# Kernel tuning notes

Measured on AMD Instinct MI355X. Metric: run time of the kernel, lower is better.

The kernel has to match this reference:

```python
import jax, jax.numpy as jnp
import numpy as np

DIM = 64  # QK head dim, matches init kwarg 'dim'

def setup_inputs() -> dict:
    key = jax.random.key(0)
    kq, kk, kv = jax.random.split(key, 3)
    B, L, C, D, H = 2, 2048, 16, DIM, 64
    query = jax.random.normal(kq, (B, L, C, D), dtype=jnp.float32)
    k_ = jax.random.normal(kk, (B, L, C, D), dtype=jnp.float32)
    value = jax.random.normal(kv, (B, L, C, H), dtype=jnp.float32)
    return {"query": query, "key": k_, "value": value}

def reference(query, key, value):
    scaler = 1.0 / jnp.sqrt(jnp.float32(DIM))
    # score: [b, c, l, m]
    score = jnp.einsum('blcd,bmcd->bclm', query, key) * scaler
    # mask=False, dropout=0 -> identity
    attn = jax.nn.softmax(score, axis=3)
    # out: [b, l, c, h]
    out = jnp.einsum('bmch,bclm->blch', value, attn)
    return out
```

## Files before the change

kernel.cpp:

```cpp
#include <hip/hip_runtime.h>
#include <hip/hip_bf16.h>
#include <stdint.h>

#define B_ 2
#define L_ 2048
#define C_ 16
#define D_ 64
#define H_ 64
#define QBLK 128
#define KVBLK 64
#define NTILES 32
#define NTHREADS 256
#define NHEADS 32
#define TILE_ELEMS 4096
#define TENSOR_ELEMS (NHEADS * NTILES * TILE_ELEMS)

typedef __attribute__((ext_vector_type(8))) short bf16x8;
typedef __attribute__((ext_vector_type(16))) float f32x16;
typedef __attribute__((ext_vector_type(8))) unsigned short u16x8;

__device__ inline unsigned short f2bf(float f) {
  union { float f; unsigned int u; } v; v.f = f;
  unsigned int u = v.u;
  unsigned int r = (u + 0x7FFFu + ((u >> 16) & 1u)) >> 16;
  return (unsigned short)r;
}

__device__ inline float fast_exp2(float x) {
#if __has_builtin(__builtin_amdgcn_exp2f)
  return __builtin_amdgcn_exp2f(x);
#else
  return exp2f(x);
#endif
}

__device__ inline unsigned cvt_pk_bf16(float lo, float hi) {
  unsigned r;
  asm("v_cvt_pk_bf16_f32 %0, %1, %2" : "=v"(r) : "v"(lo), "v"(hi));
  return r;
}

__device__ inline void pl32swap(unsigned &x, unsigned &y) {
#if __has_builtin(__builtin_amdgcn_permlane32_swap)
  auto r = __builtin_amdgcn_permlane32_swap(x, y, false, false);
  x = r[0]; y = r[1];
#else
  asm("v_permlane32_swap_b32 %0, %1" : "+v"(x), "+&v"(y));
#endif
}

__device__ inline float xsum32(float v) {
  unsigned x = __float_as_uint(v), y = x;
  pl32swap(x, y);
  return __uint_as_float(x) + __uint_as_float(y);
}

__global__ __launch_bounds__(256) void prepack_kernel(
    const float* __restrict__ Kg, const float* __restrict__ Vg,
    unsigned short* __restrict__ Kb, unsigned short* __restrict__ Vb) {
  int idx = blockIdx.x * 256 + threadIdx.x;
  if (idx < 524288) {
    int i = idx;
    int lane = i & 63, frag = (i >> 6) & 7, t = (i >> 9) & 31, head = i >> 14;
    int b = head >> 4, c = head & 15;
    int ks = frag >> 1, half = frag & 1;
    int row = half * 32 + (lane & 31);
    int kb = ks * 16 + (lane >> 5) * 8;
    const float* src = Kg + ((size_t)(b * L_ + t * 64 + row) * C_ + c) * D_ + kb;
    float4 a0 = ((const float4*)src)[0];
    float4 a1 = ((const float4*)src)[1];
    u16x8 pk;
    pk[0] = f2bf(a0.x); pk[1] = f2bf(a0.y); pk[2] = f2bf(a0.z); pk[3] = f2bf(a0.w);
    pk[4] = f2bf(a1.x); pk[5] = f2bf(a1.y); pk[6] = f2bf(a1.z); pk[7] = f2bf(a1.w);
    size_t dst = ((((size_t)(head * 32 + t)) * 8 + frag) * 64 + lane) * 8;
    *(u16x8*)&Kb[dst] = pk;
  } else {
    int i = idx - 524288;
    int lane = i & 63, frag = (i >> 6) & 7, t = (i >> 9) & 31, head = i >> 14;
    int b = head >> 4, c = head & 15;
    int m = frag >> 1, half = frag & 1;
    int h = half * 32 + (lane & 31);
    int kv0 = m * 16 + (lane >> 5) * 8;
    const float* src = Vg + ((size_t)(b * L_ + t * 64 + kv0) * C_ + c) * H_ + h;
    u16x8 pv;
#pragma unroll
    for (int j = 0; j < 8; ++j) pv[j] = f2bf(src[(size_t)j * C_ * H_]);
    size_t dst = ((((size_t)(head * 32 + t)) * 8 + frag) * 64 + lane) * 8;
    *(u16x8*)&Vb[dst] = pv;
  }
}

#define SM(S0, S1, PF, L)                                                         \
  {                                                                               \
    float rst[4];                                                                 \
    _Pragma("unroll")                                                             \
    for (int tq = 0; tq < 4; ++tq) {                                              \
      const int be = ((2 * tq) & 3) * 4;                                          \
      const int bo = ((2 * tq + 1) & 3) * 4;                                      \
      float p0[4], p1[4];                                                         \
      _Pragma("unroll")                                                           \
      for (int r = 0; r < 4; ++r) {                                               \
        float se = (tq < 2) ? S0[be + r] : S1[be + r];                            \
        float so_ = (tq < 2) ? S0[bo + r] : S1[bo + r];                           \
        p0[r] = fast_exp2(se);                                                    \
        p1[r] = fast_exp2(so_);                                                   \
      }                                                                           \
      rst[tq] = ((p0[0] + p0[1]) + (p0[2] + p0[3])) +                             \
                ((p1[0] + p1[1]) + (p1[2] + p1[3]));                              \
      unsigned x0 = cvt_pk_bf16(p0[0], p0[1]);                                    \
      unsigned x1 = cvt_pk_bf16(p0[2], p0[3]);                                    \
      unsigned y0 = cvt_pk_bf16(p1[0], p1[1]);                                    \
      unsigned y1 = cvt_pk_bf16(p1[2], p1[3]);                                    \
      pl32swap(x0, y0);                                                           \
      pl32swap(x1, y1);                                                           \
      union { unsigned wd[4]; bf16x8 v; } pk_;                                    \
      pk_.wd[0] = x0; pk_.wd[1] = x1; pk_.wd[2] = y0; pk_.wd[3] = y1;             \
      PF[tq] = pk_.v;                                                             \
    }                                                                             \
    L += (rst[0] + rst[1]) + (rst[2] + rst[3]);                                   \
  }

__global__ __launch_bounds__(NTHREADS, 2) void attn_fwd_kernel(
    const float* __restrict__ Qg,
    const unsigned short* __restrict__ Kb,
    const unsigned short* __restrict__ Vb,
    float* __restrict__ Og) {
  __shared__ float Osh[2 * 64 * 68];
  __shared__ float lsh[2 * 2 * 64];

  const int tid  = threadIdx.x;
  const int lane = tid & 63;
  const int w    = tid >> 6;
  const int qw   = w >> 1;
  const int g    = w & 1;
  const int ql   = lane & 31;
  const int u    = lane >> 5;

  const int bid   = blockIdx.x;
  const int swz   = (bid & 7) * 64 + (bid >> 3);
  const int head  = swz >> 4;
  const int qtile = swz & 15;
  const int b     = head >> 4;
  const int c     = head & 15;
  const int q0    = qtile * QBLK + qw * 64;

  const unsigned short* KbL = Kb + (size_t)head * NTILES * TILE_ELEMS + lane * 8;
  const unsigned short* VbL = Vb + (size_t)head * NTILES * TILE_ELEMS + lane * 8;

  const float sc2 = 0.125f * 1.44269504088896340736f;
  bf16x8 qf0[4], qf1[4];
#pragma unroll
  for (int h = 0; h < 2; ++h) {
    const int qr = q0 + h * 32 + ql;
    const float* qrow = Qg + ((size_t)(b * L_ + qr) * C_ + c) * D_;
#pragma unroll
    for (int ks = 0; ks < 4; ++ks) {
      float4 a0 = *(const float4*)(qrow + ks * 16 + u * 8);
      float4 a1 = *(const float4*)(qrow + ks * 16 + u * 8 + 4);
      bf16x8 q8;
      q8[0] = (short)f2bf(a0.x * sc2); q8[1] = (short)f2bf(a0.y * sc2);
      q8[2] = (short)f2bf(a0.z * sc2); q8[3] = (short)f2bf(a0.w * sc2);
      q8[4] = (short)f2bf(a1.x * sc2); q8[5] = (short)f2bf(a1.y * sc2);
      q8[6] = (short)f2bf(a1.z * sc2); q8[7] = (short)f2bf(a1.w * sc2);
      if (h == 0) qf0[ks] = q8; else qf1[ks] = q8;
    }
  }

  f32x16 o00, o01, o10, o11;
#pragma unroll
  for (int i = 0; i < 16; ++i) { o00[i] = 0.f; o01[i] = 0.f; o10[i] = 0.f; o11[i] = 0.f; }
  float l0 = 0.f, l1 = 0.f;

  bf16x8 ka0, ka1, ka2, ka3;
  {
    const unsigned short* K0 = KbL + (size_t)g * TILE_ELEMS;
    ka0 = *(const bf16x8*)(K0);
    ka1 = *(const bf16x8*)(K0 + 512);
    ka2 = *(const bf16x8*)(K0 + 1024);
    ka3 = *(const bf16x8*)(K0 + 1536);
  }

  for (int tt = 0; tt < NTILES / 2; ++tt) {
    const int t = g + 2 * tt;
    const int tn = (tt + 1 < NTILES / 2) ? t + 2 : t;
    const unsigned short* Kt = KbL + (size_t)t * TILE_ELEMS;
    const unsigned short* Vt = VbL + (size_t)t * TILE_ELEMS;
    const unsigned short* Kn = KbL + (size_t)tn * TILE_ELEMS;

    f32x16 s00, s01, s10, s11;
#pragma unroll
    for (int i = 0; i < 16; ++i) { s00[i] = 0.f; s01[i] = 0.f; s10[i] = 0.f; s11[i] = 0.f; }

    bf16x8 kb0 = *(const bf16x8*)(Kt + 2048);
    bf16x8 kb1 = *(const bf16x8*)(Kt + 2560);
    bf16x8 kb2 = *(const bf16x8*)(Kt + 3072);
    bf16x8 kb3 = *(const bf16x8*)(Kt + 3584);
    __builtin_amdgcn_s_setprio(1);
    s00 = __builtin_amdgcn_mfma_f32_32x32x16_bf16(ka0, qf0[0], s00, 0, 0, 0);
    s01 = __builtin_amdgcn_mfma_f32_32x32x16_bf16(ka1, qf0[0], s01, 0, 0, 0);
    s10 = __builtin_amdgcn_mfma_f32_32x32x16_bf16(ka0, qf1[0], s10, 0, 0, 0);
    s11 = __builtin_amdgcn_mfma_f32_32x32x16_bf16(ka1, qf1[0], s11, 0, 0, 0);
    s00 = __builtin_amdgcn_mfma_f32_32x32x16_bf16(ka2, qf0[1], s00, 0, 0, 0);
    s01 = __builtin_amdgcn_mfma_f32_32x32x16_bf16(ka3, qf0[1], s01, 0, 0, 0);
    s10 = __builtin_amdgcn_mfma_f32_32x32x16_bf16(ka2, qf1[1], s10, 0, 0, 0);
    s11 = __builtin_amdgcn_mfma_f32_32x32x16_bf16(ka3, qf1[1], s11, 0, 0, 0);
    __builtin_amdgcn_s_setprio(0);

    ka0 = *(const bf16x8*)(Vt);
    ka1 = *(const bf16x8*)(Vt + 512);
    ka2 = *(const bf16x8*)(Vt + 1024);
    ka3 = *(const bf16x8*)(Vt + 1536);
    __builtin_amdgcn_s_setprio(1);
    s00 = __builtin_amdgcn_mfma_f32_32x32x16_bf16(kb0, qf0[2], s00, 0, 0, 0);
    s01 = __builtin_amdgcn_mfma_f32_32x32x16_bf16(kb1, qf0[2], s01, 0, 0, 0);
    s10 = __builtin_amdgcn_mfma_f32_32x32x16_bf16(kb0, qf1[2], s10, 0, 0, 0);
    s11 = __builtin_amdgcn_mfma_f32_32x32x16_bf16(kb1, qf1[2], s11, 0, 0, 0);
    s00 = __builtin_amdgcn_mfma_f32_32x32x16_bf16(kb2, qf0[3], s00, 0, 0, 0);
    s01 = __builtin_amdgcn_mfma_f32_32x32x16_bf16(kb3, qf0[3], s01, 0, 0, 0);
    s10 = __builtin_amdgcn_mfma_f32_32x32x16_bf16(kb2, qf1[3], s10, 0, 0, 0);
    s11 = __builtin_amdgcn_mfma_f32_32x32x16_bf16(kb3, qf1[3], s11, 0, 0, 0);
    __builtin_amdgcn_s_setprio(0);

    kb0 = *(const bf16x8*)(Vt + 2048);
    kb1 = *(const bf16x8*)(Vt + 2560);
    kb2 = *(const bf16x8*)(Vt + 3072);
    kb3 = *(const bf16x8*)(Vt + 3584);
    bf16x8 pf0[4], pf1[4];
    SM(s00, s01, pf0, l0);
    SM(s10, s11, pf1, l1);

    __builtin_amdgcn_s_setprio(1);
    o00 = __builtin_amdgcn_mfma_f32_32x32x16_bf16(ka0, pf0[0], o00, 0, 0, 0);
    o01 = __builtin_amdgcn_mfma_f32_32x32x16_bf16(ka1, pf0[0], o01, 0, 0, 0);
    o10 = __builtin_amdgcn_mfma_f32_32x32x16_bf16(ka0, pf1[0], o10, 0, 0, 0);
    o11 = __builtin_amdgcn_mfma_f32_32x32x16_bf16(ka1, pf1[0], o11, 0, 0, 0);
    o00 = __builtin_amdgcn_mfma_f32_32x32x16_bf16(ka2, pf0[1], o00, 0, 0, 0);
    o01 = __builtin_amdgcn_mfma_f32_32x32x16_bf16(ka3, pf0[1], o01, 0, 0, 0);
    o10 = __builtin_amdgcn_mfma_f32_32x32x16_bf16(ka2, pf1[1], o10, 0, 0, 0);
    o11 = __builtin_amdgcn_mfma_f32_32x32x16_bf16(ka3, pf1[1], o11, 0, 0, 0);
    __builtin_amdgcn_s_setprio(0);

    ka0 = *(const bf16x8*)(Kn);
    ka1 = *(const bf16x8*)(Kn + 512);
    ka2 = *(const bf16x8*)(Kn + 1024);
    ka3 = *(const bf16x8*)(Kn + 1536);
    __builtin_amdgcn_s_setprio(1);
    o00 = __builtin_amdgcn_mfma_f32_32x32x16_bf16(kb0, pf0[2], o00, 0, 0, 0);
    o01 = __builtin_amdgcn_mfma_f32_32x32x16_bf16(kb1, pf0[2], o01, 0, 0, 0);
    o10 = __builtin_amdgcn_mfma_f32_32x32x16_bf16(kb0, pf1[2], o10, 0, 0, 0);
    o11 = __builtin_amdgcn_mfma_f32_32x32x16_bf16(kb1, pf1[2], o11, 0, 0, 0);
    o00 = __builtin_amdgcn_mfma_f32_32x32x16_bf16(kb2, pf0[3], o00, 0, 0, 0);
    o01 = __builtin_amdgcn_mfma_f32_32x32x16_bf16(kb3, pf0[3], o01, 0, 0, 0);
    o10 = __builtin_amdgcn_mfma_f32_32x32x16_bf16(kb2, pf1[3], o10, 0, 0, 0);
    o11 = __builtin_amdgcn_mfma_f32_32x32x16_bf16(kb3, pf1[3], o11, 0, 0, 0);
    __builtin_amdgcn_s_setprio(0);
  }

  float la0 = xsum32(l0), la1 = xsum32(l1);
  float* Ow = &Osh[(qw * 64 + lane) * 68];
  if (g == 1) {
#pragma unroll
    for (int rg = 0; rg < 4; ++rg) {
      *(float4*)(Ow + rg * 4)      = (float4){o00[rg*4+0], o00[rg*4+1], o00[rg*4+2], o00[rg*4+3]};
      *(float4*)(Ow + 16 + rg * 4) = (float4){o01[rg*4+0], o01[rg*4+1], o01[rg*4+2], o01[rg*4+3]};
      *(float4*)(Ow + 32 + rg * 4) = (float4){o10[rg*4+0], o10[rg*4+1], o10[rg*4+2], o10[rg*4+3]};
      *(float4*)(Ow + 48 + rg * 4) = (float4){o11[rg*4+0], o11[rg*4+1], o11[rg*4+2], o11[rg*4+3]};
    }
    lsh[(qw * 2 + 0) * 64 + lane] = la0;
    lsh[(qw * 2 + 1) * 64 + lane] = la1;
  }
  __syncthreads();
  if (g == 0) {
    const float inv0 = 1.0f / (la0 + lsh[(qw * 2 + 0) * 64 + lane]);
    const float inv1 = 1.0f / (la1 + lsh[(qw * 2 + 1) * 64 + lane]);
    const int qr0 = q0 + ql;
    const int qr1 = q0 + 32 + ql;
    float* orow0 = Og + ((size_t)(b * L_ + qr0) * C_ + c) * H_;
    float* orow1 = Og + ((size_t)(b * L_ + qr1) * C_ + c) * H_;
#pragma unroll
    for (int rg = 0; rg < 4; ++rg) {
      float4 a0 = *(const float4*)(Ow + rg * 4);
      float4 a1 = *(const float4*)(Ow + 16 + rg * 4);
      float4 a2 = *(const float4*)(Ow + 32 + rg * 4);
      float4 a3 = *(const float4*)(Ow + 48 + rg * 4);
      float4 v0, v1, v2, v3;
      v0.x = (o00[rg*4+0] + a0.x) * inv0; v0.y = (o00[rg*4+1] + a0.y) * inv0;
      v0.z = (o00[rg*4+2] + a0.z) * inv0; v0.w = (o00[rg*4+3] + a0.w) * inv0;
      v1.x = (o01[rg*4+0] + a1.x) * inv0; v1.y = (o01[rg*4+1] + a1.y) * inv0;
      v1.z = (o01[rg*4+2] + a1.z) * inv0; v1.w = (o01[rg*4+3] + a1.w) * inv0;
      v2.x = (o10[rg*4+0] + a2.x) * inv1; v2.y = (o10[rg*4+1] + a2.y) * inv1;
      v2.z = (o10[rg*4+2] + a2.z) * inv1; v2.w = (o10[rg*4+3] + a2.w) * inv1;
      v3.x = (o11[rg*4+0] + a3.x) * inv1; v3.y = (o11[rg*4+1] + a3.y) * inv1;
      v3.z = (o11[rg*4+2] + a3.z) * inv1; v3.w = (o11[rg*4+3] + a3.w) * inv1;
      *(float4*)(orow0 + 8 * rg + 4 * u) = v0;
      *(float4*)(orow0 + 32 + 8 * rg + 4 * u) = v1;
      *(float4*)(orow1 + 8 * rg + 4 * u) = v2;
      *(float4*)(orow1 + 32 + 8 * rg + 4 * u) = v3;
    }
  }
}

extern "C" void kernel_launch(void* const* d_in, const int* in_sizes, int n_in,
                              void* d_out, int out_size, void* d_ws, size_t ws_size,
                              hipStream_t stream) {
  const float* Qg = (const float*)d_in[0];
  const float* Kg = (const float*)d_in[1];
  const float* Vg = (const float*)d_in[2];
  float* Og = (float*)d_out;

  unsigned short* Kb = (unsigned short*)d_ws;
  unsigned short* Vb = Kb + (size_t)TENSOR_ELEMS;

  prepack_kernel<<<4096, 256, 0, stream>>>(Kg, Vg, Kb, Vb);

  dim3 grid(NHEADS * (L_ / QBLK));
  dim3 block(NTHREADS);
  attn_fwd_kernel<<<grid, block, 0, stream>>>(Qg, Kb, Vb, Og);
}
```

Baseline: 57.87 us.

## Halve query block to 64 rows per block for more blocks and occupancy

Each wave now handles 32 query rows instead of 64, so the block covers 64 queries and the grid doubles to 1024 blocks. Accumulator and score registers are halved, launch bounds are raised to 3 blocks per SIMD, and the grid swizzle and shared-memory reduction buffers are resized. The aim is more parallelism and latency hiding, at the cost of each K/V tile being reloaded from L2 by twice as many blocks and less MFMA work per load.

```diff
diff --git a/kernel.cpp b/kernel.cpp
--- a/kernel.cpp
+++ b/kernel.cpp
@@ -7,7 +7,7 @@
 #define C_ 16
 #define D_ 64
 #define H_ 64
-#define QBLK 128
+#define QBLK 64
 #define KVBLK 64
 #define NTILES 32
 #define NTHREADS 256
@@ -120,13 +120,13 @@
     L += (rst[0] + rst[1]) + (rst[2] + rst[3]);                                   \
   }
 
-__global__ __launch_bounds__(NTHREADS, 2) void attn_fwd_kernel(
+__global__ __launch_bounds__(NTHREADS, 3) void attn_fwd_kernel(
     const float* __restrict__ Qg,
     const unsigned short* __restrict__ Kb,
     const unsigned short* __restrict__ Vb,
     float* __restrict__ Og) {
-  __shared__ float Osh[2 * 64 * 68];
-  __shared__ float lsh[2 * 2 * 64];
+  __shared__ float Osh[2 * 64 * 36];
+  __shared__ float lsh[2 * 64];
 
   const int tid  = threadIdx.x;
   const int lane = tid & 63;
@@ -137,39 +137,36 @@
   const int u    = lane >> 5;
 
   const int bid   = blockIdx.x;
-  const int swz   = (bid & 7) * 64 + (bid >> 3);
-  const int head  = swz >> 4;
-  const int qtile = swz & 15;
+  const int swz   = (bid & 7) * 128 + (bid >> 3);
+  const int head  = swz >> 5;
+  const int qtile = swz & 31;
   const int b     = head >> 4;
   const int c     = head & 15;
-  const int q0    = qtile * QBLK + qw * 64;
+  const int q0    = qtile * QBLK + qw * 32;
 
   const unsigned short* KbL = Kb + (size_t)head * NTILES * TILE_ELEMS + lane * 8;
   const unsigned short* VbL = Vb + (size_t)head * NTILES * TILE_ELEMS + lane * 8;
 
   const float sc2 = 0.125f * 1.44269504088896340736f;
-  bf16x8 qf0[4], qf1[4];
-#pragma unroll
-  for (int h = 0; h < 2; ++h) {
-    const int qr = q0 + h * 32 + ql;
-    const float* qrow = Qg + ((size_t)(b * L_ + qr) * C_ + c) * D_;
-#pragma unroll
-    for (int ks = 0; ks < 4; ++ks) {
-      float4 a0 = *(const float4*)(qrow + ks * 16 + u * 8);
-      float4 a1 = *(const float4*)(qrow + ks * 16 + u * 8 + 4);
-      bf16x8 q8;
-      q8[0] = (short)f2bf(a0.x * sc2); q8[1] = (short)f2bf(a0.y * sc2);
-      q8[2] = (short)f2bf(a0.z * sc2); q8[3] = (short)f2bf(a0.w * sc2);
-      q8[4] = (short)f2bf(a1.x * sc2); q8[5] = (short)f2bf(a1.y * sc2);
-      q8[6] = (short)f2bf(a1.z * sc2); q8[7] = (short)f2bf(a1.w * sc2);
-      if (h == 0) qf0[ks] = q8; else qf1[ks] = q8;
-    }
-  }
-
-  f32x16 o00, o01, o10, o11;
-#pragma unroll
-  for (int i = 0; i < 16; ++i) { o00[i] = 0.f; o01[i] = 0.f; o10[i] = 0.f; o11[i] = 0.f; }
-  float l0 = 0.f, l1 = 0.f;
+  const int qr = q0 + ql;
+  const float* qrow = Qg + ((size_t)(b * L_ + qr) * C_ + c) * D_;
+  bf16x8 qf[4];
+#pragma unroll
+  for (int ks = 0; ks < 4; ++ks) {
+    float4 a0 = *(const float4*)(qrow + ks * 16 + u * 8);
+    float4 a1 = *(const float4*)(qrow + ks * 16 + u * 8 + 4);
+    bf16x8 q8;
+    q8[0] = (short)f2bf(a0.x * sc2); q8[1] = (short)f2bf(a0.y * sc2);
+    q8[2] = (short)f2bf(a0.z * sc2); q8[3] = (short)f2bf(a0.w * sc2);
+    q8[4] = (short)f2bf(a1.x * sc2); q8[5] = (short)f2bf(a1.y * sc2);
+    q8[6] = (short)f2bf(a1.z * sc2); q8[7] = (short)f2bf(a1.w * sc2);
+    qf[ks] = q8;
+  }
+
+  f32x16 o0, o1;
+#pragma unroll
+  for (int i = 0; i < 16; ++i) { o0[i] = 0.f; o1[i] = 0.f; }
+  float l_own = 0.f;
 
   bf16x8 ka0, ka1, ka2, ka3;
   {
@@ -187,23 +184,19 @@
     const unsigned short* Vt = VbL + (size_t)t * TILE_ELEMS;
     const unsigned short* Kn = KbL + (size_t)tn * TILE_ELEMS;
 
-    f32x16 s00, s01, s10, s11;
-#pragma unroll
-    for (int i = 0; i < 16; ++i) { s00[i] = 0.f; s01[i] = 0.f; s10[i] = 0.f; s11[i] = 0.f; }
+    f32x16 s0, s1;
+#pragma unroll
+    for (int i = 0; i < 16; ++i) { s0[i] = 0.f; s1[i] = 0.f; }
 
     bf16x8 kb0 = *(const bf16x8*)(Kt + 2048);
     bf16x8 kb1 = *(const bf16x8*)(Kt + 2560);
     bf16x8 kb2 = *(const bf16x8*)(Kt + 3072);
     bf16x8 kb3 = *(const bf16x8*)(Kt + 3584);
     __builtin_amdgcn_s_setprio(1);
-    s00 = __builtin_amdgcn_mfma_f32_32x32x16_bf16(ka0, qf0[0], s00, 0, 0, 0);
-    s01 = __builtin_amdgcn_mfma_f32_32x32x16_bf16(ka1, qf0[0], s01, 0, 0, 0);
-    s10 = __builtin_amdgcn_mfma_f32_32x32x16_bf16(ka0, qf1[0], s10, 0, 0, 0);
-    s11 = __builtin_amdgcn_mfma_f32_32x32x16_bf16(ka1, qf1[0], s11, 0, 0, 0);
-    s00 = __builtin_amdgcn_mfma_f32_32x32x16_bf16(ka2, qf0[1], s00, 0, 0, 0);
-    s01 = __builtin_amdgcn_mfma_f32_32x32x16_bf16(ka3, qf0[1], s01, 0, 0, 0);
-    s10 = __builtin_amdgcn_mfma_f32_32x32x16_bf16(ka2, qf1[1], s10, 0, 0, 0);
-    s11 = __builtin_amdgcn_mfma_f32_32x32x16_bf16(ka3, qf1[1], s11, 0, 0, 0);
+    s0 = __builtin_amdgcn_mfma_f32_32x32x16_bf16(ka0, qf[0], s0, 0, 0, 0);
+    s1 = __builtin_amdgcn_mfma_f32_32x32x16_bf16(ka1, qf[0], s1, 0, 0, 0);
+    s0 = __builtin_amdgcn_mfma_f32_32x32x16_bf16(ka2, qf[1], s0, 0, 0, 0);
+    s1 = __builtin_amdgcn_mfma_f32_32x32x16_bf16(ka3, qf[1], s1, 0, 0, 0);
     __builtin_amdgcn_s_setprio(0);
 
     ka0 = *(const bf16x8*)(Vt);
@@ -211,33 +204,24 @@
     ka2 = *(const bf16x8*)(Vt + 1024);
     ka3 = *(const bf16x8*)(Vt + 1536);
     __builtin_amdgcn_s_setprio(1);
-    s00 = __builtin_amdgcn_mfma_f32_32x32x16_bf16(kb0, qf0[2], s00, 0, 0, 0);
-    s01 = __builtin_amdgcn_mfma_f32_32x32x16_bf16(kb1, qf0[2], s01, 0, 0, 0);
-    s10 = __builtin_amdgcn_mfma_f32_32x32x16_bf16(kb0, qf1[2], s10, 0, 0, 0);
-    s11 = __builtin_amdgcn_mfma_f32_32x32x16_bf16(kb1, qf1[2], s11, 0, 0, 0);
-    s00 = __builtin_amdgcn_mfma_f32_32x32x16_bf16(kb2, qf0[3], s00, 0, 0, 0);
-    s01 = __builtin_amdgcn_mfma_f32_32x32x16_bf16(kb3, qf0[3], s01, 0, 0, 0);
-    s10 = __builtin_amdgcn_mfma_f32_32x32x16_bf16(kb2, qf1[3], s10, 0, 0, 0);
-    s11 = __builtin_amdgcn_mfma_f32_32x32x16_bf16(kb3, qf1[3], s11, 0, 0, 0);
+    s0 = __builtin_amdgcn_mfma_f32_32x32x16_bf16(kb0, qf[2], s0, 0, 0, 0);
+    s1 = __builtin_amdgcn_mfma_f32_32x32x16_bf16(kb1, qf[2], s1, 0, 0, 0);
+    s0 = __builtin_amdgcn_mfma_f32_32x32x16_bf16(kb2, qf[3], s0, 0, 0, 0);
+    s1 = __builtin_amdgcn_mfma_f32_32x32x16_bf16(kb3, qf[3], s1, 0, 0, 0);
     __builtin_amdgcn_s_setprio(0);
 
     kb0 = *(const bf16x8*)(Vt + 2048);
     kb1 = *(const bf16x8*)(Vt + 2560);
     kb2 = *(const bf16x8*)(Vt + 3072);
     kb3 = *(const bf16x8*)(Vt + 3584);
-    bf16x8 pf0[4], pf1[4];
-    SM(s00, s01, pf0, l0);
-    SM(s10, s11, pf1, l1);
-
-    __builtin_amdgcn_s_setprio(1);
-    o00 = __builtin_amdgcn_mfma_f32_32x32x16_bf16(ka0, pf0[0], o00, 0, 0, 0);
-    o01 = __builtin_amdgcn_mfma_f32_32x32x16_bf16(ka1, pf0[0], o01, 0, 0, 0);
-    o10 = __builtin_amdgcn_mfma_f32_32x32x16_bf16(ka0, pf1[0], o10, 0, 0, 0);
-    o11 = __builtin_amdgcn_mfma_f32_32x32x16_bf16(ka1, pf1[0], o11, 0, 0, 0);
-    o00 = __builtin_amdgcn_mfma_f32_32x32x16_bf16(ka2, pf0[1], o00, 0, 0, 0);
-    o01 = __builtin_amdgcn_mfma_f32_32x32x16_bf16(ka3, pf0[1], o01, 0, 0, 0);
-    o10 = __builtin_amdgcn_mfma_f32_32x32x16_bf16(ka2, pf1[1], o10, 0, 0, 0);
-    o11 = __builtin_amdgcn_mfma_f32_32x32x16_bf16(ka3, pf1[1], o11, 0, 0, 0);
+    bf16x8 pf[4];
+    SM(s0, s1, pf, l_own);
+
+    __builtin_amdgcn_s_setprio(1);
+    o0 = __builtin_amdgcn_mfma_f32_32x32x16_bf16(ka0, pf[0], o0, 0, 0, 0);
+    o1 = __builtin_amdgcn_mfma_f32_32x32x16_bf16(ka1, pf[0], o1, 0, 0, 0);
+    o0 = __builtin_amdgcn_mfma_f32_32x32x16_bf16(ka2, pf[1], o0, 0, 0, 0);
+    o1 = __builtin_amdgcn_mfma_f32_32x32x16_bf16(ka3, pf[1], o1, 0, 0, 0);
     __builtin_amdgcn_s_setprio(0);
 
     ka0 = *(const bf16x8*)(Kn);
@@ -245,57 +229,38 @@
     ka2 = *(const bf16x8*)(Kn + 1024);
     ka3 = *(const bf16x8*)(Kn + 1536);
     __builtin_amdgcn_s_setprio(1);
-    o00 = __builtin_amdgcn_mfma_f32_32x32x16_bf16(kb0, pf0[2], o00, 0, 0, 0);
-    o01 = __builtin_amdgcn_mfma_f32_32x32x16_bf16(kb1, pf0[2], o01, 0, 0, 0);
-    o10 = __builtin_amdgcn_mfma_f32_32x32x16_bf16(kb0, pf1[2], o10, 0, 0, 0);
-    o11 = __builtin_amdgcn_mfma_f32_32x32x16_bf16(kb1, pf1[2], o11, 0, 0, 0);
-    o00 = __builtin_amdgcn_mfma_f32_32x32x16_bf16(kb2, pf0[3], o00, 0, 0, 0);
-    o01 = __builtin_amdgcn_mfma_f32_32x32x16_bf16(kb3, pf0[3], o01, 0, 0, 0);
-    o10 = __builtin_amdgcn_mfma_f32_32x32x16_bf16(kb2, pf1[3], o10, 0, 0, 0);
-    o11 = __builtin_amdgcn_mfma_f32_32x32x16_bf16(kb3, pf1[3], o11, 0, 0, 0);
-    __builtin_amdgcn_s_setprio(0);
-  }
-
-  float la0 = xsum32(l0), la1 = xsum32(l1);
-  float* Ow = &Osh[(qw * 64 + lane) * 68];
+    o0 = __builtin_amdgcn_mfma_f32_32x32x16_bf16(kb0, pf[2], o0, 0, 0, 0);
+    o1 = __builtin_amdgcn_mfma_f32_32x32x16_bf16(kb1, pf[2], o1, 0, 0, 0);
+    o0 = __builtin_amdgcn_mfma_f32_32x32x16_bf16(kb2, pf[3], o0, 0, 0, 0);
+    o1 = __builtin_amdgcn_mfma_f32_32x32x16_bf16(kb3, pf[3], o1, 0, 0, 0);
+    __builtin_amdgcn_s_setprio(0);
+  }
+
+  float l_all = xsum32(l_own);
+  float* Ow = &Osh[(qw * 64 + lane) * 36];
   if (g == 1) {
 #pragma unroll
     for (int rg = 0; rg < 4; ++rg) {
-      *(float4*)(Ow + rg * 4)      = (float4){o00[rg*4+0], o00[rg*4+1], o00[rg*4+2], o00[rg*4+3]};
-      *(float4*)(Ow + 16 + rg * 4) = (float4){o01[rg*4+0], o01[rg*4+1], o01[rg*4+2], o01[rg*4+3]};
-      *(float4*)(Ow + 32 + rg * 4) = (float4){o10[rg*4+0], o10[rg*4+1], o10[rg*4+2], o10[rg*4+3]};
-      *(float4*)(Ow + 48 + rg * 4) = (float4){o11[rg*4+0], o11[rg*4+1], o11[rg*4+2], o11[rg*4+3]};
+      *(float4*)(Ow + rg * 4)      = (float4){o0[rg*4+0], o0[rg*4+1], o0[rg*4+2], o0[rg*4+3]};
+      *(float4*)(Ow + 16 + rg * 4) = (float4){o1[rg*4+0], o1[rg*4+1], o1[rg*4+2], o1[rg*4+3]};
     }
-    lsh[(qw * 2 + 0) * 64 + lane] = la0;
-    lsh[(qw * 2 + 1) * 64 + lane] = la1;
+    lsh[qw * 64 + lane] = l_all;
   }
   __syncthreads();
   if (g == 0) {
-    const float inv0 = 1.0f / (la0 + lsh[(qw * 2 + 0) * 64 + lane]);
-    const float inv1 = 1.0f / (la1 + lsh[(qw * 2 + 1) * 64 + lane]);
-    const int qr0 = q0 + ql;
-    const int qr1 = q0 + 32 + ql;
-    float* orow0 = Og + ((size_t)(b * L_ + qr0) * C_ + c) * H_;
-    float* orow1 = Og + ((size_t)(b * L_ + qr1) * C_ + c) * H_;
+    const float inv = 1.0f / (l_all + lsh[qw * 64 + lane]);
+    float* orow = Og + ((size_t)(b * L_ + qr) * C_ + c) * H_;
 #pragma unroll
     for (int rg = 0; rg < 4; ++rg) {
       float4 a0 = *(const float4*)(Ow + rg * 4);
       float4 a1 = *(const float4*)(Ow + 16 + rg * 4);
-      float4 a2 = *(const float4*)(Ow + 32 + rg * 4);
-      float4 a3 = *(const float4*)(Ow + 48 + rg * 4);
-      float4 v0, v1, v2, v3;
-      v0.x = (o00[rg*4+0] + a0.x) * inv0; v0.y = (o00[rg*4+1] + a0.y) * inv0;
-      v0.z = (o00[rg*4+2] + a0.z) * inv0; v0.w = (o00[rg*4+3] + a0.w) * inv0;
-      v1.x = (o01[rg*4+0] + a1.x) * inv0; v1.y = (o01[rg*4+1] + a1.y) * inv0;
-      v1.z = (o01[rg*4+2] + a1.z) * inv0; v1.w = (o01[rg*4+3] + a1.w) * inv0;
-      v2.x = (o10[rg*4+0] + a2.x) * inv1; v2.y = (o10[rg*4+1] + a2.y) * inv1;
-      v2.z = (o10[rg*4+2] + a2.z) * inv1; v2.w = (o10[rg*4+3] + a2.w) * inv1;
-      v3.x = (o11[rg*4+0] + a3.x) * inv1; v3.y = (o11[rg*4+1] + a3.y) * inv1;
-      v3.z = (o11[rg*4+2] + a3.z) * inv1; v3.w = (o11[rg*4+3] + a3.w) * inv1;
-      *(float4*)(orow0 + 8 * rg + 4 * u) = v0;
-      *(float4*)(orow0 + 32 + 8 * rg + 4 * u) = v1;
-      *(float4*)(orow1 + 8 * rg + 4 * u) = v2;
-      *(float4*)(orow1 + 32 + 8 * rg + 4 * u) = v3;
+      float4 v0, v1;
+      v0.x = (o0[rg*4+0] + a0.x) * inv; v0.y = (o0[rg*4+1] + a0.y) * inv;
+      v0.z = (o0[rg*4+2] + a0.z) * inv; v0.w = (o0[rg*4+3] + a0.w) * inv;
+      v1.x = (o1[rg*4+0] + a1.x) * inv; v1.y = (o1[rg*4+1] + a1.y) * inv;
+      v1.z = (o1[rg*4+2] + a1.z) * inv; v1.w = (o1[rg*4+3] + a1.w) * inv;
+      *(float4*)(orow + 8 * rg + 4 * u) = v0;
+      *(float4*)(orow + 32 + 8 * rg + 4 * u) = v1;
     }
   }
 }
```

New measurement: 60.28 us. 4.2% more time.
